# Kernel optimization log

Hardware: AMD Instinct MI355X
Metric: run time of the kernel (lower is better)

Reference implementation:

```python
import jax, jax.numpy as jnp
import numpy as np

KERNEL = 5
DILATIONS = (3, 1)
N_HEADS = 8
LN_EPS = 1e-5


def unfold1d(x, kernel, dilation, pad):
    # x: (N, H, S) -> (N, H, S, kernel) dilated sliding windows (same length)
    xp = jnp.pad(x, ((0, 0), (0, 0), (pad, pad)))
    S = x.shape[-1]
    idx = jnp.arange(S)[:, None] + jnp.arange(kernel)[None, :] * dilation  # (S, K)
    return xp[:, :, idx]  # (N, H, S, K)


def dilated_mha(q, k, v, Ws, bs, Wo, bo):
    # q,k,v: (B, S, D); Ws: (2, split, split); Wo: (D, D)
    B, S, D = q.shape
    ndil = len(DILATIONS)
    hpd = N_HEADS // ndil            # heads per dilation
    dk = D // N_HEADS
    split = D // ndil
    scale = dk ** (-0.5)
    outs, probs = [], []
    for i, dil in enumerate(DILATIONS):
        pad = dil * (KERNEL - 1) // 2
        sl = slice(i * split, (i + 1) * split)
        qi = q[..., sl] @ Ws[i].T + bs[i]
        ki = k[..., sl] @ Ws[i].T + bs[i]
        vi = v[..., sl] @ Ws[i].T + bs[i]
        # (B,S,hpd,dk) -> (B,dk,hpd,S), matching torch transpose(1,2).permute(0,3,1,2)
        to4 = lambda x: jnp.transpose(x.reshape(B, S, hpd, dk), (0, 3, 2, 1))
        qi4, ki4, vi4 = to4(qi), to4(ki), to4(vi)
        # unfold then reinterpret (B*dk,hpd,...) as (B*hpd,dk,...) exactly as torch .reshape does
        kp = unfold1d(ki4.reshape(B * dk, hpd, S), KERNEL, dil, pad).reshape(B * hpd, dk, S, KERNEL)
        vp = unfold1d(vi4.reshape(B * dk, hpd, S), KERNEL, dil, pad).reshape(B * hpd, dk, S, KERNEL)
        qr = qi4.reshape(B * hpd, dk, S)
        scores = jnp.einsum('nds,ndsk->nsk', qr, kp) * scale   # (B*hpd, S, K)
        p = jax.nn.softmax(scores, axis=-1)
        out = jnp.einsum('nsk,ndsk->nds', p, vp)               # (B*hpd, dk, S)
        out = jnp.transpose(out.reshape(B, hpd, dk, S), (0, 3, 1, 2)).reshape(B, S, split)
        outs.append(out)
        probs.append(p.reshape(B, hpd, S, KERNEL))
    o = jnp.concatenate(outs, axis=-1) @ Wo.T + bo
    return o, jnp.concatenate(probs, axis=1)


def layer_norm(x, g, b):
    mu = jnp.mean(x, axis=-1, keepdims=True)
    var = jnp.mean((x - mu) ** 2, axis=-1, keepdims=True)
    return (x - mu) * jax.lax.rsqrt(var + LN_EPS) * g + b


def setup_inputs() -> dict:
    key = jax.random.key(0)
    ks = jax.random.split(key, 6)
    B, S, D = 32, 2048, 256
    split = D // 2
    q_emb = jax.random.normal(ks[0], (B, S, D), dtype=jnp.float32)
    s_emb = jax.random.normal(ks[1], (B, S, D), dtype=jnp.float32)
    lens = jax.random.randint(ks[2], (B,), 5, S, dtype=jnp.int32)
    W_lin = jax.random.normal(ks[3], (3, 2, split, split), dtype=jnp.float32) * (split ** -0.5)
    b_lin = jnp.zeros((3, 2, split), dtype=jnp.float32)
    W_out = jax.random.normal(ks[4], (3, D, D), dtype=jnp.float32) * (D ** -0.5)
    b_out = jnp.zeros((3, D), dtype=jnp.float32)
    ln_g = jnp.ones((3, D), dtype=jnp.float32)
    ln_b = jnp.zeros((3, D), dtype=jnp.float32)
    return {"q_emb": q_emb, "s_emb": s_emb, "lens": lens, "W_lin": W_lin,
            "b_lin": b_lin, "W_out": W_out, "b_out": b_out, "ln_g": ln_g, "ln_b": ln_b}


def reference(q_emb, s_emb, lens, W_lin, b_lin, W_out, b_out, ln_g, ln_b):
    # CASTransformer.forward, shortcut=True path, eval mode (dropout=id, mask unused)
    a1, _ = dilated_mha(q_emb, q_emb, q_emb, W_lin[0], b_lin[0], W_out[0], b_out[0])
    hq = layer_norm(q_emb + a1, ln_g[0], ln_b[0])
    a2, q_scores = dilated_mha(s_emb, s_emb, s_emb, W_lin[1], b_lin[1], W_out[1], b_out[1])
    hs = layer_norm(s_emb + a2, ln_g[1], ln_b[1])
    a3, _ = dilated_mha(hq, hq, hs, W_lin[2], b_lin[2], W_out[2], b_out[2])
    z = layer_norm(hq + a3, ln_g[2], ln_b[2])
    return z, q_scores
```

## Files before the change

kernel.cpp:

```cpp
#include <hip/hip_runtime.h>
#include <hip/hip_bf16.h>

typedef __bf16 bf16x8 __attribute__((ext_vector_type(8)));
typedef float  f32x4  __attribute__((ext_vector_type(4)));
typedef unsigned int u32;
typedef u32 u32x4 __attribute__((ext_vector_type(4)));
typedef unsigned short ushort_t;

__device__ inline float bf2f(ushort_t h) {
    union { u32 u; float f; } v; v.u = ((u32)h) << 16; return v.f;
}
__device__ inline ushort_t f2bf(float f) {
    union { float f; u32 u; } v; v.f = f;
    u32 u = v.u;
    return (ushort_t)((u + 0x7fffu + ((u >> 16) & 1u)) >> 16);
}
__device__ inline bf16x8 load_bf8(const ushort_t* p) {
    u32x4 u = *reinterpret_cast<const u32x4*>(p);
    return __builtin_bit_cast(bf16x8, u);
}
__device__ inline bf16x8 load8_in(const void* base, size_t idx, int f32flag) {
    if (!f32flag) return load_bf8((const ushort_t*)base + idx);
    const float* pf = (const float*)base + idx;
    f32x4 a = *reinterpret_cast<const f32x4*>(pf);
    f32x4 b = *reinterpret_cast<const f32x4*>(pf + 4);
    bf16x8 r;
#pragma unroll
    for (int j = 0; j < 4; ++j) { r[j] = (__bf16)a[j]; r[4 + j] = (__bf16)b[j]; }
    return r;
}
__device__ inline float ld_in(const void* base, size_t idx, int f32flag) {
    return f32flag ? ((const float*)base)[idx] : bf2f(((const ushort_t*)base)[idx]);
}

__device__ inline int pofs(int row, int ch) { return row * 256 + (ch ^ ((row & 15) << 3)); }
__device__ inline int tofs(int tr, int ch) { return tr * 256 + (ch ^ (((tr + 8) & 15) << 3)); }

__device__ inline int f_of(const int* flags, int i) { return i < 0 ? 0 : flags[i]; }
__device__ inline int out_f32(const int* flags) {
    return flags[0] | flags[1] | flags[3] | flags[4] | flags[5] | flags[6] | flags[7] | flags[8];
}

__global__ __launch_bounds__(256) void detect_all(
    const u32* a0, const u32* a1, const u32* a2, const u32* a3,
    const u32* a4, const u32* a5, const u32* a6, const u32* a7,
    int* __restrict__ flags)
{
    const u32* arrs[8] = {a0, a1, a2, a3, a4, a5, a6, a7};
    const int  ns[8]   = {16384, 16384, 16384, 384, 16384, 384, 384, 384};
    const int  fi[8]   = {0, 1, 3, 4, 5, 6, 7, 8};
    const int  b = blockIdx.x;
    const u32* d = arrs[b];
    const int  n = ns[b];

    const int t = threadIdx.x;
    int cn = 0, co = 0;
    for (int i = t; i < n; i += 256) {
        const u32 w = d[i];
        const u32 e  = (w >> 7) & 0xFF;
        const u32 fe = (w >> 23) & 0xFF;
        cn += (e >= 100 && e <= 135) ? 1 : 0;
        co += (((w & 0xFFFFu) == 0u) && fe >= 100 && fe <= 140) ? 1 : 0;
    }
    __shared__ int sn[256], so[256];
    sn[t] = cn; so[t] = co; __syncthreads();
    for (int o = 128; o; o >>= 1) {
        if (t < o) { sn[t] += sn[t + o]; so[t] += so[t + o]; }
        __syncthreads();
    }
    if (t == 0) {
        const int CN = sn[0], CO = so[0];
        const int is_f32 = (2 * CN < n) && ((2 * CO > n) || (20 * CN > n));
        flags[fi[b]] = is_f32 ? 1 : 0;
    }
}

__global__ __launch_bounds__(256, 4) void proj2_kernel(
    const void* X0, int xi0, size_t lw0, size_t lb0, ushort_t* __restrict__ Y0,
    const void* X1, int xi1, size_t lw1, size_t lb1, ushort_t* __restrict__ Y1,
    const void* __restrict__ W, const void* __restrict__ Bv, const int* __restrict__ flags)
{
    __shared__ __align__(16) ushort_t tile[64 * 256];
    const int half = blockIdx.x >> 10;
    const void* X = half ? X1 : X0;
    const int   xi = half ? xi1 : xi0;
    const size_t lw = half ? lw1 : lw0;
    const size_t lb = half ? lb1 : lb0;
    ushort_t* Y = half ? Y1 : Y0;

    const int xf  = f_of(flags, xi);
    const int wf  = flags[3], bfl = flags[4];
    const int tid = threadIdx.x;
    const int m0  = (blockIdx.x & 1023) * 64;

#pragma unroll
    for (int i = 0; i < 8; ++i) {
        const int c = tid + 256 * i;
        const int row = c >> 5, cc = c & 31;
        bf16x8 v = load8_in(X, (size_t)(m0 + row) * 256 + cc * 8, xf);
        *reinterpret_cast<u32x4*>(&tile[pofs(row, cc * 8)]) = __builtin_bit_cast(u32x4, v);
    }
    __syncthreads();

    const int wave = tid >> 6, lane = tid & 63;
    const int dil  = wave >> 1;
    const int n_off = (wave & 1) * 64;
    const int l15  = lane & 15, quad = lane >> 4;

    f32x4 acc[4][4] = {};
    for (int kc = 0; kc < 4; ++kc) {
        bf16x8 a[4], b[4];
#pragma unroll
        for (int mt = 0; mt < 4; ++mt)
            a[mt] = load_bf8(&tile[pofs(mt * 16 + l15, dil * 128 + kc * 32 + quad * 8)]);
#pragma unroll
        for (int nt = 0; nt < 4; ++nt)
            b[nt] = load8_in(W, lw + (size_t)dil * 16384 +
                             (size_t)(n_off + nt * 16 + l15) * 128 + kc * 32 + quad * 8, wf);
#pragma unroll
        for (int mt = 0; mt < 4; ++mt)
#pragma unroll
            for (int nt = 0; nt < 4; ++nt)
                acc[mt][nt] = __builtin_amdgcn_mfma_f32_16x16x32_bf16(a[mt], b[nt], acc[mt][nt], 0, 0, 0);
    }
    __syncthreads();

#pragma unroll
    for (int nt = 0; nt < 4; ++nt) {
        const int ncol = n_off + nt * 16 + l15;
        const float bias = ld_in(Bv, lb + dil * 128 + ncol, bfl);
#pragma unroll
        for (int mt = 0; mt < 4; ++mt)
#pragma unroll
            for (int r = 0; r < 4; ++r) {
                const int row = mt * 16 + quad * 4 + r;
                tile[pofs(row, dil * 128 + ncol)] = f2bf(acc[mt][nt][r] + bias);
            }
    }
    __syncthreads();

#pragma unroll
    for (int i = 0; i < 8; ++i) {
        const int c = tid + 256 * i;
        const int row = c >> 5, cc = c & 31;
        *reinterpret_cast<u32x4*>(Y + (size_t)(m0 + row) * 256 + cc * 8) =
            *reinterpret_cast<const u32x4*>(&tile[row * 256 + cc * 8]);
    }
}

__global__ __launch_bounds__(256, 4) void fused2_kernel(
    const ushort_t* P0, const ushort_t* V0, const void* R0, int ri0,
    size_t lw0, size_t lb0, size_t lg0, void* H0, int h0, void* pr0,
    const ushort_t* P1, const ushort_t* V1, const void* R1, int ri1,
    size_t lw1, size_t lb1, size_t lg1, void* H1, int h1, void* pr1,
    const void* __restrict__ W, const void* __restrict__ Bv,
    const void* __restrict__ G, const void* __restrict__ Bt,
    const int* __restrict__ flags)
{
    __shared__ __align__(16) ushort_t tile[80 * 256];
    float (*lsum)[64] = (float (*)[64])(&tile[0]);
    float (*lsq)[64]  = (float (*)[64])(&tile[1024]);

    const int half = blockIdx.x >> 10;
    const ushort_t* P = half ? P1 : P0;
    const ushort_t* V = half ? V1 : V0;
    const void* R  = half ? R1 : R0;
    const int   ri = half ? ri1 : ri0;
    const size_t lw = half ? lw1 : lw0;
    const size_t lb = half ? lb1 : lb0;
    const size_t lg = half ? lg1 : lg0;
    void* H        = half ? H1 : H0;
    const int h_out = half ? h1 : h0;
    void* probs_base = half ? pr1 : pr0;

    const int wf = flags[5], bvf = flags[6], gf = flags[7], btf = flags[8];
    const int rf = f_of(flags, ri);
    const int og = out_f32(flags);
    const int of = h_out ? og : 0;

    const int tid  = threadIdx.x;
    const int wave = tid >> 6, lane = tid & 63;
    const int l15  = lane & 15, quad = lane >> 4;
    const int m0   = (blockIdx.x & 1023) * 64;
    const int bb   = m0 >> 11;
    const int s0   = m0 & 2047;
    const size_t rowbase = (size_t)bb * 2048;
    const float scale = 0.17677669529663687f;

#pragma unroll
    for (int i = 0; i < 10; ++i) {
        const int c = tid + 256 * i;
        const int tr = c >> 5, cc = c & 31;
        int s = s0 - 8 + tr; s = s < 0 ? 0 : (s > 2047 ? 2047 : s);
        *reinterpret_cast<u32x4*>(&tile[tr * 256 + cc * 8]) =
            *reinterpret_cast<const u32x4*>(P + (rowbase + s) * 256 + cc * 8);
    }
    __syncthreads();

    const int r = lane, g = wave;
    const int s = s0 + r;

    float p2[2][5];
#pragma unroll
    for (int it = 0; it < 2; ++it) {
        const int dil  = it;
        const int dila = dil ? 1 : 3;
        const int ch0  = dil * 128 + g * 8;

        float qv[4][8];
#pragma unroll
        for (int h = 0; h < 4; ++h) {
            bf16x8 t = load_bf8(&tile[tofs(8 + r, ch0 + h * 32)]);
#pragma unroll
            for (int j = 0; j < 8; ++j) qv[h][j] = (float)t[j];
        }
        float sc[5];
#pragma unroll
        for (int kk = 0; kk < 5; ++kk) {
            const int sp = s + (kk - 2) * dila;
            float a = 0.f;
            if (sp >= 0 && sp < 2048) {
                const int tr2 = 8 + r + (kk - 2) * dila;
#pragma unroll
                for (int h = 0; h < 4; ++h) {
                    bf16x8 t = load_bf8(&tile[tofs(tr2, ch0 + h * 32)]);
#pragma unroll
                    for (int j = 0; j < 8; ++j) a += qv[h][j] * (float)t[j];
                }
                a *= scale;
            }
            sc[kk] = a;
        }
        float mx = sc[0];
#pragma unroll
        for (int kk = 1; kk < 5; ++kk) mx = fmaxf(mx, sc[kk]);
        float sum = 0.f;
#pragma unroll
        for (int kk = 0; kk < 5; ++kk) { p2[it][kk] = __expf(sc[kk] - mx); sum += p2[it][kk]; }
        const float inv = 1.f / sum;
#pragma unroll
        for (int kk = 0; kk < 5; ++kk) p2[it][kk] *= inv;

        if (probs_base != nullptr) {
            const size_t pb = 16777216 + ((size_t)((bb * 8 + dil * 4 + g) * 2048 + s)) * 5;
            if (og) {
                float* pp = (float*)probs_base;
#pragma unroll
                for (int kk = 0; kk < 5; ++kk) pp[pb + kk] = p2[it][kk];
            } else {
                ushort_t* pp = (ushort_t*)probs_base;
#pragma unroll
                for (int kk = 0; kk < 5; ++kk) pp[pb + kk] = f2bf(p2[it][kk]);
            }
        }
    }

    if (V != P) {
        __syncthreads();
#pragma unroll
        for (int i = 0; i < 10; ++i) {
            const int c = tid + 256 * i;
            const int tr = c >> 5, cc = c & 31;
            int s2 = s0 - 8 + tr; s2 = s2 < 0 ? 0 : (s2 > 2047 ? 2047 : s2);
            *reinterpret_cast<u32x4*>(&tile[tr * 256 + cc * 8]) =
                *reinterpret_cast<const u32x4*>(V + (rowbase + s2) * 256 + cc * 8);
        }
        __syncthreads();
    }

    u32x4 wpk[2][4];
#pragma unroll
    for (int it = 0; it < 2; ++it) {
        const int dil  = it;
        const int dila = dil ? 1 : 3;
        const int ch0  = dil * 128 + g * 8;
        float o[4][8] = {};
#pragma unroll
        for (int kk = 0; kk < 5; ++kk) {
            const int sp = s + (kk - 2) * dila;
            if (sp < 0 || sp >= 2048) continue;
            const int tr2 = 8 + r + (kk - 2) * dila;
#pragma unroll
            for (int h = 0; h < 4; ++h) {
                bf16x8 t = load_bf8(&tile[tofs(tr2, ch0 + h * 32)]);
#pragma unroll
                for (int j = 0; j < 8; ++j) o[h][j] += p2[it][kk] * (float)t[j];
            }
        }
#pragma unroll
        for (int c = 0; c < 4; ++c) {
            u32x4 w;
#pragma unroll
            for (int t4 = 0; t4 < 4; ++t4) {
                const int d2a = c * 8 + t4 * 2, d2b = d2a + 1;
                const u32 lo = f2bf(o[d2a & 3][d2a >> 2]);
                const u32 hi = f2bf(o[d2b & 3][d2b >> 2]);
                w[t4] = lo | (hi << 16);
            }
            wpk[it][c] = w;
        }
    }
    __syncthreads();

#pragma unroll
    for (int it = 0; it < 2; ++it)
#pragma unroll
        for (int c = 0; c < 4; ++c)
            *reinterpret_cast<u32x4*>(&tile[tofs(8 + r, it * 128 + g * 32 + c * 8)]) = wpk[it][c];
    __syncthreads();

    const int n_off = wave * 64;

    f32x4 acc[4][4] = {};
    for (int kc = 0; kc < 8; ++kc) {
        bf16x8 a[4], b[4];
#pragma unroll
        for (int mt = 0; mt < 4; ++mt)
            a[mt] = load_bf8(&tile[tofs(8 + mt * 16 + l15, kc * 32 + quad * 8)]);
#pragma unroll
        for (int nt = 0; nt < 4; ++nt)
            b[nt] = load8_in(W, lw + (size_t)(n_off + nt * 16 + l15) * 256 + kc * 32 + quad * 8, wf);
#pragma unroll
        for (int mt = 0; mt < 4; ++mt)
#pragma unroll
            for (int nt = 0; nt < 4; ++nt)
                acc[mt][nt] = __builtin_amdgcn_mfma_f32_16x16x32_bf16(a[mt], b[nt], acc[mt][nt], 0, 0, 0);
    }

    float bias[4];
#pragma unroll
    for (int nt = 0; nt < 4; ++nt) bias[nt] = ld_in(Bv, lb + n_off + nt * 16 + l15, bvf);

    float psum[4][4] = {}, psq[4][4] = {};
#pragma unroll
    for (int mt = 0; mt < 4; ++mt) {
#pragma unroll
        for (int rr = 0; rr < 4; ++rr) {
            const size_t rrow = (size_t)(m0 + mt * 16 + quad * 4 + rr) * 256 + l15;
#pragma unroll
            for (int nt = 0; nt < 4; ++nt) {
                float v = acc[mt][nt][rr] + bias[nt] + ld_in(R, rrow + n_off + nt * 16, rf);
                acc[mt][nt][rr] = v;
                psum[mt][rr] += v;
                psq[mt][rr]  += v * v;
            }
        }
    }
#pragma unroll
    for (int off = 1; off <= 8; off <<= 1) {
#pragma unroll
        for (int mt = 0; mt < 4; ++mt)
#pragma unroll
            for (int rr = 0; rr < 4; ++rr) {
                psum[mt][rr] += __shfl_xor(psum[mt][rr], off);
                psq[mt][rr]  += __shfl_xor(psq[mt][rr],  off);
            }
    }
    if (l15 == 0) {
#pragma unroll
        for (int mt = 0; mt < 4; ++mt)
#pragma unroll
            for (int rr = 0; rr < 4; ++rr) {
                const int row = mt * 16 + quad * 4 + rr;
                lsum[wave][row] = psum[mt][rr];
                lsq[wave][row]  = psq[mt][rr];
            }
    }
    __syncthreads();

    float gl[4], blv[4];
#pragma unroll
    for (int nt = 0; nt < 4; ++nt) {
        gl[nt]  = ld_in(G,  lg + n_off + nt * 16 + l15, gf);
        blv[nt] = ld_in(Bt, lg + n_off + nt * 16 + l15, btf);
    }
#pragma unroll
    for (int mt = 0; mt < 4; ++mt) {
#pragma unroll
        for (int rr = 0; rr < 4; ++rr) {
            const int row = mt * 16 + quad * 4 + rr;
            const float sm = lsum[0][row] + lsum[1][row] + lsum[2][row] + lsum[3][row];
            const float q2 = lsq[0][row]  + lsq[1][row]  + lsq[2][row]  + lsq[3][row];
            const float mu  = sm * (1.f / 256.f);
            const float var = q2 * (1.f / 256.f) - mu * mu;
            const float rs  = rsqrtf(var + 1e-5f);
#pragma unroll
            for (int nt = 0; nt < 4; ++nt)
                acc[mt][nt][rr] = (acc[mt][nt][rr] - mu) * rs * gl[nt] + blv[nt];
        }
    }
    __syncthreads();

    if (of) {
        float* tf = (float*)tile;
#pragma unroll
        for (int hh = 0; hh < 2; ++hh) {
#pragma unroll
            for (int mh = 0; mh < 2; ++mh) {
                const int mt = 2 * hh + mh;
#pragma unroll
                for (int rr = 0; rr < 4; ++rr) {
                    const int lrow = mh * 16 + quad * 4 + rr;
#pragma unroll
                    for (int nt = 0; nt < 4; ++nt)
                        tf[lrow * 256 + n_off + nt * 16 + l15] = acc[mt][nt][rr];
                }
            }
            __syncthreads();
#pragma unroll
            for (int i = 0; i < 8; ++i) {
                const int c = tid + 256 * i;
                const int row = c >> 6, cc = c & 63;
                *reinterpret_cast<f32x4*>((float*)H + (size_t)(m0 + hh * 32 + row) * 256 + cc * 4) =
                    *reinterpret_cast<const f32x4*>(&tf[row * 256 + cc * 4]);
            }
            __syncthreads();
        }
    } else {
#pragma unroll
        for (int mt = 0; mt < 4; ++mt)
#pragma unroll
            for (int rr = 0; rr < 4; ++rr) {
                const int row = mt * 16 + quad * 4 + rr;
#pragma unroll
                for (int nt = 0; nt < 4; ++nt)
                    tile[pofs(row, n_off + nt * 16 + l15)] = f2bf(acc[mt][nt][rr]);
            }
        __syncthreads();
#pragma unroll
        for (int i = 0; i < 8; ++i) {
            const int c = tid + 256 * i;
            const int row = c >> 5, cc = c & 31;
            const int sc8 = (cc * 8) ^ ((row & 15) << 3);
            *reinterpret_cast<u32x4*>((ushort_t*)H + (size_t)(m0 + row) * 256 + cc * 8) =
                *reinterpret_cast<const u32x4*>(&tile[row * 256 + sc8]);
        }
    }
}

extern "C" void kernel_launch(void* const* d_in, const int* in_sizes, int n_in,
                              void* d_out, int out_size, void* d_ws, size_t ws_size,
                              hipStream_t stream) {
    const void* q_emb = d_in[0];
    const void* s_emb = d_in[1];
    const void* W_lin = d_in[3];
    const void* b_lin = d_in[4];
    const void* W_out = d_in[5];
    const void* b_out = d_in[6];
    const void* ln_g  = d_in[7];
    const void* ln_b  = d_in[8];

    const size_t SLOT = 16777216;
    int*      flags = (int*)d_ws;
    ushort_t* S1 = (ushort_t*)((char*)d_ws + 256);
    ushort_t* S2 = S1 + SLOT;
    ushort_t* S3 = S1 + 2 * SLOT;
    ushort_t* S4 = S1 + 3 * SLOT;
    const size_t need4 = 256 + 4 * SLOT * sizeof(ushort_t);

    const dim3 blk(256);
    detect_all<<<8, blk, 0, stream>>>((const u32*)q_emb, (const u32*)s_emb, (const u32*)W_lin,
        (const u32*)b_lin, (const u32*)W_out, (const u32*)b_out,
        (const u32*)ln_g, (const u32*)ln_b, flags);

    proj2_kernel<<<2048, blk, 0, stream>>>(q_emb, 0, 0, 0, S1,
                                           s_emb, 1, 32768, 256, S2,
                                           W_lin, b_lin, flags);

    if (ws_size >= need4) {
        fused2_kernel<<<2048, blk, 0, stream>>>(
            S1, S1, q_emb, 0, 0,     0,   0,   S3, 0, nullptr,
            S2, S2, s_emb, 1, 65536, 256, 256, S4, 0, d_out,
            W_out, b_out, ln_g, ln_b, flags);
        proj2_kernel<<<2048, blk, 0, stream>>>(S3, -1, 65536, 512, S1,
                                               S4, -1, 65536, 512, S2,
                                               W_lin, b_lin, flags);
        fused2_kernel<<<1024, blk, 0, stream>>>(
            S1, S2, S3, -1, 131072, 512, 512, d_out, 1, nullptr,
            S1, S2, S3, -1, 131072, 512, 512, d_out, 1, nullptr,
            W_out, b_out, ln_g, ln_b, flags);
    } else {
        fused2_kernel<<<1024, blk, 0, stream>>>(
            S1, S1, q_emb, 0, 0, 0, 0, S3, 0, nullptr,
            S1, S1, q_emb, 0, 0, 0, 0, S3, 0, nullptr,
            W_out, b_out, ln_g, ln_b, flags);
        fused2_kernel<<<1024, blk, 0, stream>>>(
            S2, S2, s_emb, 1, 65536, 256, 256, S1, 0, d_out,
            S2, S2, s_emb, 1, 65536, 256, 256, S1, 0, d_out,
            W_out, b_out, ln_g, ln_b, flags);
        proj2_kernel<<<2048, blk, 0, stream>>>(S3, -1, 65536, 512, S2,
                                               S1, -1, 65536, 512, S1,
                                               W_lin, b_lin, flags);
        fused2_kernel<<<1024, blk, 0, stream>>>(
            S2, S1, S3, -1, 131072, 512, 512, d_out, 1, nullptr,
            S2, S1, S3, -1, 131072, 512, 512, d_out, 1, nullptr,
            W_out, b_out, ln_g, ln_b, flags);
    }
}
```

Baseline: 571.0 us.

## Halve row tile to 32, remap attention threads, prefetch V into registers

Both the projection and fused attention kernels now process 32 rows per block instead of 64, which halves shared memory and accumulator registers and doubles the grid. Launch bounds are raised to allow more resident blocks per CU. In the fused kernel, each thread now handles one (dilation, head-group, row) triple instead of looping over both dilations. The separate V tile is loaded into registers early so its global latency overlaps the score computation. The trade-off is twice as many blocks and more halo rows reloaded relative to useful rows, while the weight matrix is reused over fewer rows per load.

```diff
diff --git a/kernel.cpp b/kernel.cpp
--- a/kernel.cpp
+++ b/kernel.cpp
@@ -75,13 +75,13 @@
     }
 }
 
-__global__ __launch_bounds__(256, 4) void proj2_kernel(
+__global__ __launch_bounds__(256, 8) void proj2_kernel(
     const void* X0, int xi0, size_t lw0, size_t lb0, ushort_t* __restrict__ Y0,
     const void* X1, int xi1, size_t lw1, size_t lb1, ushort_t* __restrict__ Y1,
     const void* __restrict__ W, const void* __restrict__ Bv, const int* __restrict__ flags)
 {
-    __shared__ __align__(16) ushort_t tile[64 * 256];
-    const int half = blockIdx.x >> 10;
+    __shared__ __align__(16) ushort_t tile[32 * 256];
+    const int half = blockIdx.x >> 11;
     const void* X = half ? X1 : X0;
     const int   xi = half ? xi1 : xi0;
     const size_t lw = half ? lw1 : lw0;
@@ -91,10 +91,10 @@
     const int xf  = f_of(flags, xi);
     const int wf  = flags[3], bfl = flags[4];
     const int tid = threadIdx.x;
-    const int m0  = (blockIdx.x & 1023) * 64;
-
-#pragma unroll
-    for (int i = 0; i < 8; ++i) {
+    const int m0  = (blockIdx.x & 2047) * 32;
+
+#pragma unroll
+    for (int i = 0; i < 4; ++i) {
         const int c = tid + 256 * i;
         const int row = c >> 5, cc = c & 31;
         bf16x8 v = load8_in(X, (size_t)(m0 + row) * 256 + cc * 8, xf);
@@ -107,18 +107,18 @@
     const int n_off = (wave & 1) * 64;
     const int l15  = lane & 15, quad = lane >> 4;
 
-    f32x4 acc[4][4] = {};
+    f32x4 acc[2][4] = {};
     for (int kc = 0; kc < 4; ++kc) {
-        bf16x8 a[4], b[4];
-#pragma unroll
-        for (int mt = 0; mt < 4; ++mt)
+        bf16x8 a[2], b[4];
+#pragma unroll
+        for (int mt = 0; mt < 2; ++mt)
             a[mt] = load_bf8(&tile[pofs(mt * 16 + l15, dil * 128 + kc * 32 + quad * 8)]);
 #pragma unroll
         for (int nt = 0; nt < 4; ++nt)
             b[nt] = load8_in(W, lw + (size_t)dil * 16384 +
                              (size_t)(n_off + nt * 16 + l15) * 128 + kc * 32 + quad * 8, wf);
 #pragma unroll
-        for (int mt = 0; mt < 4; ++mt)
+        for (int mt = 0; mt < 2; ++mt)
 #pragma unroll
             for (int nt = 0; nt < 4; ++nt)
                 acc[mt][nt] = __builtin_amdgcn_mfma_f32_16x16x32_bf16(a[mt], b[nt], acc[mt][nt], 0, 0, 0);
@@ -130,7 +130,7 @@
         const int ncol = n_off + nt * 16 + l15;
         const float bias = ld_in(Bv, lb + dil * 128 + ncol, bfl);
 #pragma unroll
-        for (int mt = 0; mt < 4; ++mt)
+        for (int mt = 0; mt < 2; ++mt)
 #pragma unroll
             for (int r = 0; r < 4; ++r) {
                 const int row = mt * 16 + quad * 4 + r;
@@ -140,7 +140,7 @@
     __syncthreads();
 
 #pragma unroll
-    for (int i = 0; i < 8; ++i) {
+    for (int i = 0; i < 4; ++i) {
         const int c = tid + 256 * i;
         const int row = c >> 5, cc = c & 31;
         *reinterpret_cast<u32x4*>(Y + (size_t)(m0 + row) * 256 + cc * 8) =
@@ -148,7 +148,7 @@
     }
 }
 
-__global__ __launch_bounds__(256, 4) void fused2_kernel(
+__global__ __launch_bounds__(256, 6) void fused2_kernel(
     const ushort_t* P0, const ushort_t* V0, const void* R0, int ri0,
     size_t lw0, size_t lb0, size_t lg0, void* H0, int h0, void* pr0,
     const ushort_t* P1, const ushort_t* V1, const void* R1, int ri1,
@@ -157,11 +157,11 @@
     const void* __restrict__ G, const void* __restrict__ Bt,
     const int* __restrict__ flags)
 {
-    __shared__ __align__(16) ushort_t tile[80 * 256];
-    float (*lsum)[64] = (float (*)[64])(&tile[0]);
-    float (*lsq)[64]  = (float (*)[64])(&tile[1024]);
-
-    const int half = blockIdx.x >> 10;
+    __shared__ __align__(16) ushort_t tile[48 * 256];
+    float (*lsum)[32] = (float (*)[32])(&tile[0]);
+    float (*lsq)[32]  = (float (*)[32])(&tile[256]);
+
+    const int half = blockIdx.x >> 11;
     const ushort_t* P = half ? P1 : P0;
     const ushort_t* V = half ? V1 : V0;
     const void* R  = half ? R1 : R0;
@@ -181,14 +181,14 @@
     const int tid  = threadIdx.x;
     const int wave = tid >> 6, lane = tid & 63;
     const int l15  = lane & 15, quad = lane >> 4;
-    const int m0   = (blockIdx.x & 1023) * 64;
+    const int m0   = (blockIdx.x & 2047) * 32;
     const int bb   = m0 >> 11;
     const int s0   = m0 & 2047;
     const size_t rowbase = (size_t)bb * 2048;
     const float scale = 0.17677669529663687f;
 
 #pragma unroll
-    for (int i = 0; i < 10; ++i) {
+    for (int i = 0; i < 6; ++i) {
         const int c = tid + 256 * i;
         const int tr = c >> 5, cc = c & 31;
         int s = s0 - 8 + tr; s = s < 0 ? 0 : (s > 2047 ? 2047 : s);
@@ -197,131 +197,129 @@
     }
     __syncthreads();
 
-    const int r = lane, g = wave;
-    const int s = s0 + r;
-
-    float p2[2][5];
-#pragma unroll
-    for (int it = 0; it < 2; ++it) {
-        const int dil  = it;
-        const int dila = dil ? 1 : 3;
-        const int ch0  = dil * 128 + g * 8;
-
-        float qv[4][8];
-#pragma unroll
-        for (int h = 0; h < 4; ++h) {
-            bf16x8 t = load_bf8(&tile[tofs(8 + r, ch0 + h * 32)]);
-#pragma unroll
-            for (int j = 0; j < 8; ++j) qv[h][j] = (float)t[j];
-        }
-        float sc[5];
-#pragma unroll
-        for (int kk = 0; kk < 5; ++kk) {
-            const int sp = s + (kk - 2) * dila;
-            float a = 0.f;
-            if (sp >= 0 && sp < 2048) {
-                const int tr2 = 8 + r + (kk - 2) * dila;
-#pragma unroll
-                for (int h = 0; h < 4; ++h) {
-                    bf16x8 t = load_bf8(&tile[tofs(tr2, ch0 + h * 32)]);
-#pragma unroll
-                    for (int j = 0; j < 8; ++j) a += qv[h][j] * (float)t[j];
-                }
-                a *= scale;
-            }
-            sc[kk] = a;
-        }
-        float mx = sc[0];
-#pragma unroll
-        for (int kk = 1; kk < 5; ++kk) mx = fmaxf(mx, sc[kk]);
-        float sum = 0.f;
-#pragma unroll
-        for (int kk = 0; kk < 5; ++kk) { p2[it][kk] = __expf(sc[kk] - mx); sum += p2[it][kk]; }
-        const float inv = 1.f / sum;
-#pragma unroll
-        for (int kk = 0; kk < 5; ++kk) p2[it][kk] *= inv;
-
-        if (probs_base != nullptr) {
-            const size_t pb = 16777216 + ((size_t)((bb * 8 + dil * 4 + g) * 2048 + s)) * 5;
-            if (og) {
-                float* pp = (float*)probs_base;
-#pragma unroll
-                for (int kk = 0; kk < 5; ++kk) pp[pb + kk] = p2[it][kk];
-            } else {
-                ushort_t* pp = (ushort_t*)probs_base;
-#pragma unroll
-                for (int kk = 0; kk < 5; ++kk) pp[pb + kk] = f2bf(p2[it][kk]);
-            }
-        }
-    }
-
-    if (V != P) {
-        __syncthreads();
-#pragma unroll
-        for (int i = 0; i < 10; ++i) {
+    const int dg  = tid >> 5;
+    const int dil = dg >> 2, g = dg & 3;
+    const int r   = tid & 31;
+    const int dila = dil ? 1 : 3;
+    const int ch0  = dil * 128 + g * 8;
+    const int s    = s0 + r;
+
+    const bool sepv = (V != P);
+    u32x4 vstg[6];
+    if (sepv) {
+#pragma unroll
+        for (int i = 0; i < 6; ++i) {
             const int c = tid + 256 * i;
             const int tr = c >> 5, cc = c & 31;
             int s2 = s0 - 8 + tr; s2 = s2 < 0 ? 0 : (s2 > 2047 ? 2047 : s2);
-            *reinterpret_cast<u32x4*>(&tile[tr * 256 + cc * 8]) =
-                *reinterpret_cast<const u32x4*>(V + (rowbase + s2) * 256 + cc * 8);
-        }
-        __syncthreads();
-    }
-
-    u32x4 wpk[2][4];
-#pragma unroll
-    for (int it = 0; it < 2; ++it) {
-        const int dil  = it;
-        const int dila = dil ? 1 : 3;
-        const int ch0  = dil * 128 + g * 8;
-        float o[4][8] = {};
-#pragma unroll
-        for (int kk = 0; kk < 5; ++kk) {
-            const int sp = s + (kk - 2) * dila;
-            if (sp < 0 || sp >= 2048) continue;
+            vstg[i] = *reinterpret_cast<const u32x4*>(V + (rowbase + s2) * 256 + cc * 8);
+        }
+    }
+
+    float qv[4][8];
+#pragma unroll
+    for (int h = 0; h < 4; ++h) {
+        bf16x8 t = load_bf8(&tile[tofs(8 + r, ch0 + h * 32)]);
+#pragma unroll
+        for (int j = 0; j < 8; ++j) qv[h][j] = (float)t[j];
+    }
+    float sc[5];
+#pragma unroll
+    for (int kk = 0; kk < 5; ++kk) {
+        const int sp = s + (kk - 2) * dila;
+        float a = 0.f;
+        if (sp >= 0 && sp < 2048) {
             const int tr2 = 8 + r + (kk - 2) * dila;
 #pragma unroll
             for (int h = 0; h < 4; ++h) {
                 bf16x8 t = load_bf8(&tile[tofs(tr2, ch0 + h * 32)]);
 #pragma unroll
-                for (int j = 0; j < 8; ++j) o[h][j] += p2[it][kk] * (float)t[j];
-            }
-        }
-#pragma unroll
-        for (int c = 0; c < 4; ++c) {
-            u32x4 w;
-#pragma unroll
-            for (int t4 = 0; t4 < 4; ++t4) {
-                const int d2a = c * 8 + t4 * 2, d2b = d2a + 1;
-                const u32 lo = f2bf(o[d2a & 3][d2a >> 2]);
-                const u32 hi = f2bf(o[d2b & 3][d2b >> 2]);
-                w[t4] = lo | (hi << 16);
-            }
-            wpk[it][c] = w;
-        }
-    }
-    __syncthreads();
-
-#pragma unroll
-    for (int it = 0; it < 2; ++it)
-#pragma unroll
-        for (int c = 0; c < 4; ++c)
-            *reinterpret_cast<u32x4*>(&tile[tofs(8 + r, it * 128 + g * 32 + c * 8)]) = wpk[it][c];
+                for (int j = 0; j < 8; ++j) a += qv[h][j] * (float)t[j];
+            }
+            a *= scale;
+        }
+        sc[kk] = a;
+    }
+    float mx = sc[0];
+#pragma unroll
+    for (int kk = 1; kk < 5; ++kk) mx = fmaxf(mx, sc[kk]);
+    float p[5], sum = 0.f;
+#pragma unroll
+    for (int kk = 0; kk < 5; ++kk) { p[kk] = __expf(sc[kk] - mx); sum += p[kk]; }
+    const float inv = 1.f / sum;
+#pragma unroll
+    for (int kk = 0; kk < 5; ++kk) p[kk] *= inv;
+
+    if (probs_base != nullptr) {
+        const size_t pb = 16777216 + ((size_t)((bb * 8 + dg) * 2048 + s)) * 5;
+        if (og) {
+            float* pp = (float*)probs_base;
+#pragma unroll
+            for (int kk = 0; kk < 5; ++kk) pp[pb + kk] = p[kk];
+        } else {
+            ushort_t* pp = (ushort_t*)probs_base;
+#pragma unroll
+            for (int kk = 0; kk < 5; ++kk) pp[pb + kk] = f2bf(p[kk]);
+        }
+    }
+
+    if (sepv) {
+        __syncthreads();
+#pragma unroll
+        for (int i = 0; i < 6; ++i) {
+            const int c = tid + 256 * i;
+            const int tr = c >> 5, cc = c & 31;
+            *reinterpret_cast<u32x4*>(&tile[tr * 256 + cc * 8]) = vstg[i];
+        }
+        __syncthreads();
+    }
+
+    float o[4][8] = {};
+#pragma unroll
+    for (int kk = 0; kk < 5; ++kk) {
+        const int sp = s + (kk - 2) * dila;
+        if (sp < 0 || sp >= 2048) continue;
+        const int tr2 = 8 + r + (kk - 2) * dila;
+#pragma unroll
+        for (int h = 0; h < 4; ++h) {
+            bf16x8 t = load_bf8(&tile[tofs(tr2, ch0 + h * 32)]);
+#pragma unroll
+            for (int j = 0; j < 8; ++j) o[h][j] += p[kk] * (float)t[j];
+        }
+    }
+    u32x4 wpk[4];
+#pragma unroll
+    for (int c = 0; c < 4; ++c) {
+        u32x4 w;
+#pragma unroll
+        for (int t4 = 0; t4 < 4; ++t4) {
+            const int d2a = c * 8 + t4 * 2, d2b = d2a + 1;
+            const u32 lo = f2bf(o[d2a & 3][d2a >> 2]);
+            const u32 hi = f2bf(o[d2b & 3][d2b >> 2]);
+            w[t4] = lo | (hi << 16);
+        }
+        wpk[c] = w;
+    }
+    __syncthreads();
+
+#pragma unroll
+    for (int c = 0; c < 4; ++c)
+        *reinterpret_cast<u32x4*>(&tile[tofs(8 + r, dil * 128 + g * 32 + c * 8)]) = wpk[c];
     __syncthreads();
 
     const int n_off = wave * 64;
 
-    f32x4 acc[4][4] = {};
+    f32x4 acc[2][4] = {};
     for (int kc = 0; kc < 8; ++kc) {
-        bf16x8 a[4], b[4];
-#pragma unroll
-        for (int mt = 0; mt < 4; ++mt)
+        bf16x8 a[2], b[4];
+#pragma unroll
+        for (int mt = 0; mt < 2; ++mt)
             a[mt] = load_bf8(&tile[tofs(8 + mt * 16 + l15, kc * 32 + quad * 8)]);
 #pragma unroll
         for (int nt = 0; nt < 4; ++nt)
             b[nt] = load8_in(W, lw + (size_t)(n_off + nt * 16 + l15) * 256 + kc * 32 + quad * 8, wf);
 #pragma unroll
-        for (int mt = 0; mt < 4; ++mt)
+        for (int mt = 0; mt < 2; ++mt)
 #pragma unroll
             for (int nt = 0; nt < 4; ++nt)
                 acc[mt][nt] = __builtin_amdgcn_mfma_f32_16x16x32_bf16(a[mt], b[nt], acc[mt][nt], 0, 0, 0);
@@ -331,9 +329,9 @@
 #pragma unroll
     for (int nt = 0; nt < 4; ++nt) bias[nt] = ld_in(Bv, lb + n_off + nt * 16 + l15, bvf);
 
-    float psum[4][4] = {}, psq[4][4] = {};
-#pragma unroll
-    for (int mt = 0; mt < 4; ++mt) {
+    float psum[2][4] = {}, psq[2][4] = {};
+#pragma unroll
+    for (int mt = 0; mt < 2; ++mt) {
 #pragma unroll
         for (int rr = 0; rr < 4; ++rr) {
             const size_t rrow = (size_t)(m0 + mt * 16 + quad * 4 + rr) * 256 + l15;
@@ -349,7 +347,7 @@
 #pragma unroll
     for (int off = 1; off <= 8; off <<= 1) {
 #pragma unroll
-        for (int mt = 0; mt < 4; ++mt)
+        for (int mt = 0; mt < 2; ++mt)
 #pragma unroll
             for (int rr = 0; rr < 4; ++rr) {
                 psum[mt][rr] += __shfl_xor(psum[mt][rr], off);
@@ -358,7 +356,7 @@
     }
     if (l15 == 0) {
 #pragma unroll
-        for (int mt = 0; mt < 4; ++mt)
+        for (int mt = 0; mt < 2; ++mt)
 #pragma unroll
             for (int rr = 0; rr < 4; ++rr) {
                 const int row = mt * 16 + quad * 4 + rr;
@@ -375,7 +373,7 @@
         blv[nt] = ld_in(Bt, lg + n_off + nt * 16 + l15, btf);
     }
 #pragma unroll
-    for (int mt = 0; mt < 4; ++mt) {
+    for (int mt = 0; mt < 2; ++mt) {
 #pragma unroll
         for (int rr = 0; rr < 4; ++rr) {
             const int row = mt * 16 + quad * 4 + rr;
@@ -396,29 +394,25 @@
 #pragma unroll
         for (int hh = 0; hh < 2; ++hh) {
 #pragma unroll
-            for (int mh = 0; mh < 2; ++mh) {
-                const int mt = 2 * hh + mh;
-#pragma unroll
-                for (int rr = 0; rr < 4; ++rr) {
-                    const int lrow = mh * 16 + quad * 4 + rr;
-#pragma unroll
-                    for (int nt = 0; nt < 4; ++nt)
-                        tf[lrow * 256 + n_off + nt * 16 + l15] = acc[mt][nt][rr];
-                }
+            for (int rr = 0; rr < 4; ++rr) {
+                const int lrow = quad * 4 + rr;
+#pragma unroll
+                for (int nt = 0; nt < 4; ++nt)
+                    tf[lrow * 256 + n_off + nt * 16 + l15] = acc[hh][nt][rr];
             }
             __syncthreads();
 #pragma unroll
-            for (int i = 0; i < 8; ++i) {
+            for (int i = 0; i < 4; ++i) {
                 const int c = tid + 256 * i;
                 const int row = c >> 6, cc = c & 63;
-                *reinterpret_cast<f32x4*>((float*)H + (size_t)(m0 + hh * 32 + row) * 256 + cc * 4) =
+                *reinterpret_cast<f32x4*>((float*)H + (size_t)(m0 + hh * 16 + row) * 256 + cc * 4) =
                     *reinterpret_cast<const f32x4*>(&tf[row * 256 + cc * 4]);
             }
             __syncthreads();
         }
     } else {
 #pragma unroll
-        for (int mt = 0; mt < 4; ++mt)
+        for (int mt = 0; mt < 2; ++mt)
 #pragma unroll
             for (int rr = 0; rr < 4; ++rr) {
                 const int row = mt * 16 + quad * 4 + rr;
@@ -428,7 +422,7 @@
             }
         __syncthreads();
 #pragma unroll
-        for (int i = 0; i < 8; ++i) {
+        for (int i = 0; i < 4; ++i) {
             const int c = tid + 256 * i;
             const int row = c >> 5, cc = c & 31;
             const int sc8 = (cc * 8) ^ ((row & 15) << 3);
@@ -463,35 +457,35 @@
         (const u32*)b_lin, (const u32*)W_out, (const u32*)b_out,
         (const u32*)ln_g, (const u32*)ln_b, flags);
 
-    proj2_kernel<<<2048, blk, 0, stream>>>(q_emb, 0, 0, 0, S1,
+    proj2_kernel<<<4096, blk, 0, stream>>>(q_emb, 0, 0, 0, S1,
                                            s_emb, 1, 32768, 256, S2,
                                            W_lin, b_lin, flags);
 
     if (ws_size >= need4) {
-        fused2_kernel<<<2048, blk, 0, stream>>>(
+        fused2_kernel<<<4096, blk, 0, stream>>>(
             S1, S1, q_emb, 0, 0,     0,   0,   S3, 0, nullptr,
             S2, S2, s_emb, 1, 65536, 256, 256, S4, 0, d_out,
             W_out, b_out, ln_g, ln_b, flags);
-        proj2_kernel<<<2048, blk, 0, stream>>>(S3, -1, 65536, 512, S1,
+        proj2_kernel<<<4096, blk, 0, stream>>>(S3, -1, 65536, 512, S1,
                                                S4, -1, 65536, 512, S2,
                                                W_lin, b_lin, flags);
-        fused2_kernel<<<1024, blk, 0, stream>>>(
+        fused2_kernel<<<2048, blk, 0, stream>>>(
             S1, S2, S3, -1, 131072, 512, 512, d_out, 1, nullptr,
             S1, S2, S3, -1, 131072, 512, 512, d_out, 1, nullptr,
             W_out, b_out, ln_g, ln_b, flags);
     } else {
-        fused2_kernel<<<1024, blk, 0, stream>>>(
+        fused2_kernel<<<2048, blk, 0, stream>>>(
             S1, S1, q_emb, 0, 0, 0, 0, S3, 0, nullptr,
             S1, S1, q_emb, 0, 0, 0, 0, S3, 0, nullptr,
             W_out, b_out, ln_g, ln_b, flags);
-        fused2_kernel<<<1024, blk, 0, stream>>>(
+        fused2_kernel<<<2048, blk, 0, stream>>>(
             S2, S2, s_emb, 1, 65536, 256, 256, S1, 0, d_out,
             S2, S2, s_emb, 1, 65536, 256, 256, S1, 0, d_out,
             W_out, b_out, ln_g, ln_b, flags);
-        proj2_kernel<<<2048, blk, 0, stream>>>(S3, -1, 65536, 512, S2,
+        proj2_kernel<<<4096, blk, 0, stream>>>(S3, -1, 65536, 512, S2,
                                                S1, -1, 65536, 512, S1,
                                                W_lin, b_lin, flags);
-        fused2_kernel<<<1024, blk, 0, stream>>>(
+        fused2_kernel<<<2048, blk, 0, stream>>>(
             S2, S1, S3, -1, 131072, 512, 512, d_out, 1, nullptr,
             S2, S1, S3, -1, 131072, 512, 512, d_out, 1, nullptr,
             W_out, b_out, ln_g, ln_b, flags);
```

After: 759.2 us. 1.33x slower.
